# Optimization experiments

Hardware: AMD Instinct MI355X
Metric: run time of the kernel (lower is better)

Reference implementation:

```python
import jax, jax.numpy as jnp
import numpy as np

B, N, E = 2, 2048, 1024
H = 16
D = E // H  # head_dim = 64
MLP = 4096
EPS = 1e-5


def _layernorm(x, g, b):
    mu = jnp.mean(x, axis=-1, keepdims=True)
    var = jnp.var(x, axis=-1, keepdims=True)
    return (x - mu) * jax.lax.rsqrt(var + EPS) * g + b


def setup_inputs() -> dict:
    key = jax.random.key(0)
    ks = jax.random.split(key, 12)
    s_e = 1.0 / np.sqrt(E)
    s_m = 1.0 / np.sqrt(MLP)
    return {
        "x": jax.random.normal(ks[0], (B, N, E), jnp.float32),
        "w_qkv": jax.random.uniform(ks[1], (E, 3 * E), jnp.float32, -s_e, s_e),
        "b_qkv": jax.random.uniform(ks[2], (3 * E,), jnp.float32, -s_e, s_e),
        "w_proj": jax.random.uniform(ks[3], (E, E), jnp.float32, -s_e, s_e),
        "b_proj": jax.random.uniform(ks[4], (E,), jnp.float32, -s_e, s_e),
        "g1": jnp.ones((E,), jnp.float32),
        "beta1": jnp.zeros((E,), jnp.float32),
        "g2": jnp.ones((E,), jnp.float32),
        "beta2": jnp.zeros((E,), jnp.float32),
        "w_fc1": jax.random.uniform(ks[5], (E, MLP), jnp.float32, -s_e, s_e),
        "b_fc1": jax.random.uniform(ks[6], (MLP,), jnp.float32, -s_e, s_e),
        "w_fc2": jax.random.uniform(ks[7], (MLP, E), jnp.float32, -s_m, s_m),
        "b_fc2": jax.random.uniform(ks[8], (E,), jnp.float32, -s_m, s_m),
    }


def reference(x, w_qkv, b_qkv, w_proj, b_proj, g1, beta1, g2, beta2,
              w_fc1, b_fc1, w_fc2, b_fc2):
    scale = D ** (-0.5)
    # --- attention block (pre-norm) ---
    h = _layernorm(x, g1, beta1)
    qkv = (h @ w_qkv + b_qkv).reshape(B, N, 3, H, D)
    q, k, v = (qkv[:, :, i].transpose(0, 2, 1, 3) for i in range(3))  # [B,H,N,D]
    scores = jnp.einsum("bhnd,bhmd->bhnm", q, k) * scale  # [B,H,N,N]
    attn = jax.nn.softmax(scores, axis=-1)
    out = jnp.einsum("bhnm,bhmd->bhnd", attn, v)
    out = out.transpose(0, 2, 1, 3).reshape(B, N, E)
    x = x + (out @ w_proj + b_proj)
    # --- MLP block (pre-norm, exact GELU as in torch default) ---
    h = _layernorm(x, g2, beta2)
    h = jax.nn.gelu(h @ w_fc1 + b_fc1, approximate=False) @ w_fc2 + b_fc2
    return x + h
```

## Files before the change

kernel.cpp:

```cpp
#include <hip/hip_runtime.h>
#include <hip/hip_bf16.h>
#include <cmath>


typedef __hip_bfloat16 bf16;
typedef __bf16 bf16x8 __attribute__((ext_vector_type(8)));
typedef __bf16 bf16x4v __attribute__((ext_vector_type(4)));
typedef float  f32x4  __attribute__((ext_vector_type(4)));

#define CB 2
#define CN 2048
#define CE 1024
#define CH 16
#define CD 64
#define CMLP 4096
#define CM (CB*CN)

#define PS 136

__device__ __forceinline__ float b2f(bf16 v){ return __bfloat162float(v); }
__device__ __forceinline__ bf16  f2b(float v){ return __float2bfloat16(v); }

__device__ __forceinline__ void gl_lds16(const void* g, void* l){
  __builtin_amdgcn_global_load_lds((__attribute__((address_space(1))) void*)g,
                                   (__attribute__((address_space(3))) void*)l,
                                   16, 0, 0);
}

__global__ __launch_bounds__(256) void transpose_k(const float* __restrict__ in,
                                                   bf16* __restrict__ out,
                                                   int K, int N){
  __shared__ float tile[32][33];
  const int n0 = blockIdx.x*32, k0 = blockIdx.y*32;
  const int tx = threadIdx.x & 31;
  const int ty = threadIdx.x >> 5;
  #pragma unroll
  for(int i=0;i<32;i+=8) tile[ty+i][tx] = in[(size_t)(k0+ty+i)*N + n0+tx];
  __syncthreads();
  #pragma unroll
  for(int i=0;i<32;i+=8) out[(size_t)(n0+ty+i)*K + k0+tx] = f2b(tile[tx][ty+i]);
}

__global__ __launch_bounds__(256) void ln_k(const float* __restrict__ x,
                                            const float* __restrict__ g,
                                            const float* __restrict__ be,
                                            bf16* __restrict__ out){
  const int row = blockIdx.x;
  const int t = threadIdx.x;
  const float4 v4 = ((const float4*)(x + (size_t)row*CE))[t];
  float v[4] = {v4.x, v4.y, v4.z, v4.w};
  float s=0.f, s2=0.f;
  #pragma unroll
  for(int i=0;i<4;i++){ s+=v[i]; s2+=v[i]*v[i]; }
  #pragma unroll
  for(int off=32; off>0; off>>=1){ s += __shfl_down(s,off); s2 += __shfl_down(s2,off); }
  __shared__ float red[8];
  __shared__ float mu_s, rs_s;
  const int wv=t>>6, ln=t&63;
  if(ln==0){ red[wv]=s; red[4+wv]=s2; }
  __syncthreads();
  if(t==0){
    float S=red[0]+red[1]+red[2]+red[3], S2=red[4]+red[5]+red[6]+red[7];
    float mu=S/CE;
    mu_s=mu; rs_s=rsqrtf(S2/CE - mu*mu + 1e-5f);
  }
  __syncthreads();
  const float mu=mu_s, rs=rs_s;
  #pragma unroll
  for(int i=0;i<4;i++){
    int c=t*4+i;
    out[(size_t)row*CE+c] = f2b((v[i]-mu)*rs*g[c] + be[c]);
  }
}

#define EP_QKV 0
#define EP_RES 1
#define EP_GELU 2

template<int MODE, int BN>
__global__ __launch_bounds__(256,2) void gemm_k(
  const bf16* __restrict__ A, const bf16* __restrict__ BT,
  const float* __restrict__ bias, const float* __restrict__ res,
  float* __restrict__ Cf, bf16* __restrict__ Cb,
  bf16* __restrict__ Cq, bf16* __restrict__ Ck, bf16* __restrict__ Cv,
  int Ksz, int Nsz)
{
  constexpr int NJ = BN/32;
  __shared__ __align__(16) bf16 Alds[2][128*64];
  __shared__ __align__(16) bf16 Blds[2][BN*64];
  const int tid = threadIdx.x;
  const int wave = tid>>6, lane = tid&63;
  const int m16 = lane&15, quad = lane>>4;
  const int wi = wave>>1, wj = wave&1;

  const int lin = blockIdx.x + gridDim.x*blockIdx.y;
  const int m_idx = (lin&7) + 8*((lin>>3)&3);
  const int n_idx = lin>>5;
  const size_t m0 = (size_t)m_idx*128;
  const size_t n0 = (size_t)n_idx*BN;

  f32x4 acc[4][NJ] = {};

  const int srow8 = lane>>3;
  const int schk  = ((lane&7)^srow8)*8;
  const bf16* pA = A  + (m0 + 32*wave      + srow8)*(size_t)Ksz + schk;
  const bf16* pB = BT + (n0 + (BN/4)*wave  + srow8)*(size_t)Ksz + schk;

  auto stage = [&](int buf, const bf16* gA, const bf16* gB){
    bf16* lA = &Alds[buf][wave*2048];
    bf16* lB = &Blds[buf][wave*(BN*16)];
    #pragma unroll
    for(int j=0;j<4;j++)  gl_lds16(gA + (size_t)(j*8)*Ksz, lA + j*512);
    #pragma unroll
    for(int j=0;j<NJ;j++) gl_lds16(gB + (size_t)(j*8)*Ksz, lB + j*512);
  };
  auto compute = [&](int buf){
    #pragma unroll
    for(int w=0;w<2;w++){
      const int sw = (m16&7);
      bf16x8 af[4], bfr[NJ];
      #pragma unroll
      for(int i=0;i<4;i++){
        const int row = wi*64+16*i+m16;
        af[i] = *(const bf16x8*)(&Alds[buf][row*64 + ((w*4+quad)^sw)*8]);
      }
      #pragma unroll
      for(int j=0;j<NJ;j++){
        const int row = wj*(BN/2)+16*j+m16;
        bfr[j] = *(const bf16x8*)(&Blds[buf][row*64 + ((w*4+quad)^sw)*8]);
      }
      #pragma unroll
      for(int i=0;i<4;i++)
        #pragma unroll
        for(int j=0;j<NJ;j++)
          acc[i][j] = __builtin_amdgcn_mfma_f32_16x16x32_bf16(af[i], bfr[j], acc[i][j], 0,0,0);
    }
  };

  const int kIters = Ksz/64;
  stage(0, pA, pB); pA += 64; pB += 64;
  for(int kb=0; kb<kIters; ++kb){
    __syncthreads();
    if(kb+1<kIters){ stage((kb+1)&1, pA, pB); pA += 64; pB += 64; }
    compute(kb&1);
  }

  #pragma unroll
  for(int i=0;i<4;i++){
    #pragma unroll
    for(int j=0;j<NJ;j++){
      const int col = (int)n0 + wj*(BN/2) + 16*j + m16;
      const float bcol = bias[col];
      #pragma unroll
      for(int r=0;r<4;r++){
        const int row = (int)m0 + wi*64 + 16*i + quad*4 + r;
        float v = acc[i][j][r] + bcol;
        if constexpr (MODE==EP_QKV){
          const int b = row>>11, n = row&2047;
          const int which = col>>10, cc = col&1023;
          const int h = cc>>6, d = cc&63;
          if(which==0)      Cq[(((size_t)(b*CH+h))*CN+n)*CD + d] = f2b(v);
          else if(which==1) Ck[(((size_t)(b*CH+h))*CN+n)*CD + d] = f2b(v);
          else              Cv[(((size_t)(b*CH+h))*CD+d)*CN + n] = f2b(v);
        } else if constexpr (MODE==EP_RES){
          v += res[(size_t)row*Nsz+col];
          Cf[(size_t)row*Nsz+col] = v;
        } else {
          const float u2 = 1.5957691216f*(v + 0.044715f*v*v*v);
          v = v * (1.f/(1.f + __expf(-u2)));
          Cb[(size_t)row*Nsz+col] = f2b(v);
        }
      }
    }
  }
}

__global__ __launch_bounds__(256,2) void attn_k(
  const bf16* __restrict__ Q, const bf16* __restrict__ Kx,
  const bf16* __restrict__ Vt, bf16* __restrict__ O)
{
  const int bh = blockIdx.y;
  const int b = bh>>4, h = bh&15;
  const int tid = threadIdx.x;
  const int wave = tid>>6, lane = tid&63;
  const int m16 = lane&15, quad = lane>>4;
  const int sw = m16&7;
  const int q0 = blockIdx.x*128 + wave*32;

  const bf16* Qb = Q  + (size_t)bh*CN*CD;
  const bf16* Kb = Kx + (size_t)bh*CN*CD;
  const bf16* Vb = Vt + (size_t)bh*CD*CN;

  bf16x8 qf[2][2];
  #pragma unroll
  for(int g=0;g<2;g++){
    const bf16* qp = Qb + (size_t)(q0+g*16+m16)*CD + quad*8;
    qf[g][0] = *(const bf16x8*)(qp);
    qf[g][1] = *(const bf16x8*)(qp + 32);
  }

  float li[2] = {0.f, 0.f};
  f32x4 oacc[2][4] = {};

  __shared__ __align__(16) bf16 Klds[128*64];
  __shared__ __align__(16) bf16 Vlds[64*128];
  __shared__ __align__(16) bf16 Plds[4][32*PS];
  bf16* Pw = &Plds[wave][0];

  const int krow = wave*32 + (lane>>3);
  const int kchk = (lane&7) ^ (lane>>3);
  const bf16* pK = Kb + (size_t)krow*CD + kchk*8;
  const int vrow = wave*16 + (lane>>4);
  const bf16* pV[4];
  #pragma unroll
  for(int j=0;j<4;j++){
    const int ck = (lane&15) ^ ((j*4 + (lane>>4)) & 7);
    pV[j] = Vb + (size_t)(vrow + j*4)*CN + ck*8;
  }
  bf16* lK = Klds + wave*2048;
  bf16* lV = Vlds + wave*2048;

  for(int kt=0; kt<CN; kt+=128){
    __syncthreads();
    #pragma unroll
    for(int j=0;j<4;j++){
      gl_lds16(pK + (size_t)j*8*CD, lK + j*512);
      gl_lds16(pV[j],               lV + j*512);
      pV[j] += 128;
    }
    pK += (size_t)128*CD;
    __syncthreads();

    f32x4 sf0[8], sf1[8];
    #pragma unroll
    for(int f=0;f<8;f++){
      const bf16* kb = Klds + (f*16+m16)*64;
      bf16x8 k0 = *(const bf16x8*)(kb + ((quad   ^ sw)*8));
      bf16x8 k1 = *(const bf16x8*)(kb + (((quad+4)^ sw)*8));
      f32x4 t0 = {}, t1 = {};
      t0 = __builtin_amdgcn_mfma_f32_16x16x32_bf16(k0, qf[0][0], t0, 0,0,0);
      t0 = __builtin_amdgcn_mfma_f32_16x16x32_bf16(k1, qf[0][1], t0, 0,0,0);
      t1 = __builtin_amdgcn_mfma_f32_16x16x32_bf16(k0, qf[1][0], t1, 0,0,0);
      t1 = __builtin_amdgcn_mfma_f32_16x16x32_bf16(k1, qf[1][1], t1, 0,0,0);
      sf0[f]=t0; sf1[f]=t1;
    }
    #pragma unroll
    for(int f=0;f<8;f++){
      bf16x4v p0, p1;
      #pragma unroll
      for(int r=0;r<4;r++){
        float e0 = __expf(sf0[f][r]*0.125f); li[0]+=e0; p0[r]=(__bf16)e0;
        float e1 = __expf(sf1[f][r]*0.125f); li[1]+=e1; p1[r]=(__bf16)e1;
      }
      *(bf16x4v*)(Pw + (size_t)m16*PS       + f*16 + quad*4) = p0;
      *(bf16x4v*)(Pw + (size_t)(16+m16)*PS  + f*16 + quad*4) = p1;
    }
    asm volatile("s_waitcnt lgkmcnt(0)" ::: "memory");
    #pragma unroll
    for(int c=0;c<4;c++){
      const bf16x8 ap0 = *(const bf16x8*)(Pw + (size_t)m16*PS      + c*32 + quad*8);
      const bf16x8 ap1 = *(const bf16x8*)(Pw + (size_t)(16+m16)*PS + c*32 + quad*8);
      #pragma unroll
      for(int dt=0;dt<4;dt++){
        const int d = dt*16+m16;
        bf16x8 bv = *(const bf16x8*)(Vlds + d*128 + (((c*4+quad) ^ sw)*8));
        oacc[0][dt] = __builtin_amdgcn_mfma_f32_16x16x32_bf16(ap0, bv, oacc[0][dt], 0,0,0);
        oacc[1][dt] = __builtin_amdgcn_mfma_f32_16x16x32_bf16(ap1, bv, oacc[1][dt], 0,0,0);
      }
    }
  }
  #pragma unroll
  for(int g=0;g<2;g++){
    li[g] += __shfl_xor(li[g], 16);
    li[g] += __shfl_xor(li[g], 32);
  }
  #pragma unroll
  for(int g=0;g<2;g++){
    float linv[4];
    #pragma unroll
    for(int r=0;r<4;r++) linv[r] = 1.f / __shfl(li[g], quad*4+r);
    #pragma unroll
    for(int dt=0;dt<4;dt++){
      #pragma unroll
      for(int r=0;r<4;r++){
        const int row = q0 + g*16 + quad*4 + r;
        O[((size_t)(b*CN+row))*CE + h*CD + dt*16 + m16] = f2b(oacc[g][dt][r]*linv[r]);
      }
    }
  }
}

extern "C" void kernel_launch(void* const* d_in, const int* in_sizes, int n_in,
                              void* d_out, int out_size, void* d_ws, size_t ws_size,
                              hipStream_t stream)
{
  (void)in_sizes; (void)n_in; (void)out_size; (void)ws_size;
  const float* x     = (const float*)d_in[0];
  const float* w_qkv = (const float*)d_in[1];
  const float* b_qkv = (const float*)d_in[2];
  const float* w_proj= (const float*)d_in[3];
  const float* b_proj= (const float*)d_in[4];
  const float* g1    = (const float*)d_in[5];
  const float* be1   = (const float*)d_in[6];
  const float* g2    = (const float*)d_in[7];
  const float* be2   = (const float*)d_in[8];
  const float* w_fc1 = (const float*)d_in[9];
  const float* b_fc1 = (const float*)d_in[10];
  const float* w_fc2 = (const float*)d_in[11];
  const float* b_fc2 = (const float*)d_in[12];
  float* out = (float*)d_out;

  char* ws = (char*)d_ws;
  size_t off = 0;
  auto alloc = [&](size_t bytes)->char*{
    char* p = ws + off;
    off += (bytes + 255) & ~(size_t)255;
    return p;
  };
  bf16* wqkvT = (bf16*)alloc((size_t)3072*1024*2);
  bf16* wprojT= (bf16*)alloc((size_t)1024*1024*2);
  bf16* wfc1T = (bf16*)alloc((size_t)4096*1024*2);
  bf16* wfc2T = (bf16*)alloc((size_t)1024*4096*2);
  bf16* h1    = (bf16*)alloc((size_t)CM*CE*2);
  bf16* q     = (bf16*)alloc((size_t)CM*CE*2);
  bf16* kk    = (bf16*)alloc((size_t)CM*CE*2);
  bf16* vT    = (bf16*)alloc((size_t)CM*CE*2);
  bf16* aO    = (bf16*)alloc((size_t)CM*CE*2);
  float* x2   = (float*)alloc((size_t)CM*CE*4);
  bf16* hmlp  = q;

  transpose_k<<<dim3(3072/32,1024/32),256,0,stream>>>(w_qkv, wqkvT, 1024,3072);
  transpose_k<<<dim3(1024/32,1024/32),256,0,stream>>>(w_proj, wprojT,1024,1024);
  transpose_k<<<dim3(4096/32,1024/32),256,0,stream>>>(w_fc1, wfc1T, 1024,4096);
  transpose_k<<<dim3(1024/32,4096/32),256,0,stream>>>(w_fc2, wfc2T, 4096,1024);

  ln_k<<<CM,256,0,stream>>>(x, g1, be1, h1);
  gemm_k<EP_QKV,128><<<dim3(3072/128, CM/128),256,0,stream>>>(
      h1, wqkvT, b_qkv, nullptr, nullptr, nullptr, q, kk, vT, 1024, 3072);
  attn_k<<<dim3(CN/128, CB*CH),256,0,stream>>>(q, kk, vT, aO);
  gemm_k<EP_RES,64><<<dim3(1024/64, CM/128),256,0,stream>>>(
      aO, wprojT, b_proj, x, x2, nullptr, nullptr,nullptr,nullptr, 1024, 1024);
  ln_k<<<CM,256,0,stream>>>(x2, g2, be2, h1);
  gemm_k<EP_GELU,128><<<dim3(4096/128, CM/128),256,0,stream>>>(
      h1, wfc1T, b_fc1, nullptr, nullptr, hmlp, nullptr,nullptr,nullptr, 1024, 4096);
  gemm_k<EP_RES,64><<<dim3(1024/64, CM/128),256,0,stream>>>(
      hmlp, wfc2T, b_fc2, x2, out, nullptr, nullptr,nullptr,nullptr, 4096, 1024);
}
```

Before: 351.3 us.

## Merge weight transposes into one launch, remap attention blocks, use exp2

The four weight-transpose launches become one kernel that picks its matrix from the block index, removing three launch overheads and tail gaps. Attention blocks are remapped so that consecutive blocks interleave eight heads and the query blocks within each head, which is meant to improve K/V cache locality across the blocks running at the same time. The softmax exponent now uses the hardware exp2 builtin with the scale folded into a log2(e) constant, cutting per-element arithmetic. The block remapping relies on the fixed grid shape of 16 by 32.

```diff
diff --git a/kernel.cpp b/kernel.cpp
--- a/kernel.cpp
+++ b/kernel.cpp
@@ -18,6 +18,13 @@
 
 #define PS 136
 
+#define SM_SCALE_LOG2E 0.18033688011112042f
+#if __has_builtin(__builtin_amdgcn_exp2f)
+#define FEXP(s) __builtin_amdgcn_exp2f((s)*SM_SCALE_LOG2E)
+#else
+#define FEXP(s) __expf((s)*0.125f)
+#endif
+
 __device__ __forceinline__ float b2f(bf16 v){ return __bfloat162float(v); }
 __device__ __forceinline__ bf16  f2b(float v){ return __float2bfloat16(v); }
 
@@ -27,11 +34,20 @@
                                    16, 0, 0);
 }
 
-__global__ __launch_bounds__(256) void transpose_k(const float* __restrict__ in,
-                                                   bf16* __restrict__ out,
-                                                   int K, int N){
+__global__ __launch_bounds__(256) void transpose4_k(
+  const float* __restrict__ i0, bf16* __restrict__ o0,
+  const float* __restrict__ i1, bf16* __restrict__ o1,
+  const float* __restrict__ i2, bf16* __restrict__ o2,
+  const float* __restrict__ i3, bf16* __restrict__ o3)
+{
   __shared__ float tile[32][33];
-  const int n0 = blockIdx.x*32, k0 = blockIdx.y*32;
+  int t = blockIdx.x;
+  const float* in; bf16* out; int K, N, nx;
+  if(t < 3072){            in=i0; out=o0; K=1024; N=3072; nx=96; }
+  else if(t < 4096){ t-=3072; in=i1; out=o1; K=1024; N=1024; nx=32; }
+  else if(t < 8192){ t-=4096; in=i2; out=o2; K=1024; N=4096; nx=128; }
+  else {             t-=8192; in=i3; out=o3; K=4096; N=1024; nx=32; }
+  const int n0 = (t%nx)*32, k0 = (t/nx)*32;
   const int tx = threadIdx.x & 31;
   const int ty = threadIdx.x >> 5;
   #pragma unroll
@@ -179,13 +195,15 @@
   const bf16* __restrict__ Q, const bf16* __restrict__ Kx,
   const bf16* __restrict__ Vt, bf16* __restrict__ O)
 {
-  const int bh = blockIdx.y;
+  const int lin = blockIdx.x + gridDim.x*blockIdx.y;
+  const int bh = (lin&7) + 8*(lin>>7);
+  const int qblk = (lin>>3)&15;
   const int b = bh>>4, h = bh&15;
   const int tid = threadIdx.x;
   const int wave = tid>>6, lane = tid&63;
   const int m16 = lane&15, quad = lane>>4;
   const int sw = m16&7;
-  const int q0 = blockIdx.x*128 + wave*32;
+  const int q0 = qblk*128 + wave*32;
 
   const bf16* Qb = Q  + (size_t)bh*CN*CD;
   const bf16* Kb = Kx + (size_t)bh*CN*CD;
@@ -249,8 +267,8 @@
       bf16x4v p0, p1;
       #pragma unroll
       for(int r=0;r<4;r++){
-        float e0 = __expf(sf0[f][r]*0.125f); li[0]+=e0; p0[r]=(__bf16)e0;
-        float e1 = __expf(sf1[f][r]*0.125f); li[1]+=e1; p1[r]=(__bf16)e1;
+        float e0 = FEXP(sf0[f][r]); li[0]+=e0; p0[r]=(__bf16)e0;
+        float e1 = FEXP(sf1[f][r]); li[1]+=e1; p1[r]=(__bf16)e1;
       }
       *(bf16x4v*)(Pw + (size_t)m16*PS       + f*16 + quad*4) = p0;
       *(bf16x4v*)(Pw + (size_t)(16+m16)*PS  + f*16 + quad*4) = p1;
@@ -329,10 +347,8 @@
   float* x2   = (float*)alloc((size_t)CM*CE*4);
   bf16* hmlp  = q;
 
-  transpose_k<<<dim3(3072/32,1024/32),256,0,stream>>>(w_qkv, wqkvT, 1024,3072);
-  transpose_k<<<dim3(1024/32,1024/32),256,0,stream>>>(w_proj, wprojT,1024,1024);
-  transpose_k<<<dim3(4096/32,1024/32),256,0,stream>>>(w_fc1, wfc1T, 1024,4096);
-  transpose_k<<<dim3(1024/32,4096/32),256,0,stream>>>(w_fc2, wfc2T, 4096,1024);
+  transpose4_k<<<12288,256,0,stream>>>(w_qkv, wqkvT, w_proj, wprojT,
+                                       w_fc1, wfc1T, w_fc2, wfc2T);
 
   ln_k<<<CM,256,0,stream>>>(x, g1, be1, h1);
   gemm_k<EP_QKV,128><<<dim3(3072/128, CM/128),256,0,stream>>>(
```

Result: faster. 343.2 us (-2.3%).
